# Performance work log

Hardware: AMD Instinct MI355X
Metric: run time of the kernel (lower is better)

Reference implementation:

```python
import jax, jax.numpy as jnp
import numpy as np

N = 100000   # occupied voxels
C = 128      # input_dim
G = 64       # voxel grid extent per axis


def _build_neighbor_map(rng):
    # random unique voxel coords in a G^3 grid + hash lookup for 3x3x3 offsets
    lin = rng.choice(G ** 3, size=N, replace=False)
    coords = np.stack(np.unravel_index(lin, (G, G, G)), axis=1).astype(np.int64)  # [N,3]
    lut = np.full(G ** 3, -1, np.int32)
    lut[lin] = np.arange(N, dtype=np.int32)
    o = np.arange(-1, 2)
    offs = np.stack(np.meshgrid(o, o, o, indexing='ij'), -1).reshape(27, 3)  # [27,3]
    nc = coords[None, :, :] + offs[:, None, :]                 # [27,N,3]
    valid = ((nc >= 0) & (nc < G)).all(-1)                     # [27,N]
    nlin = (nc[..., 0] * G + nc[..., 1]) * G + nc[..., 2]
    nbr = np.where(valid, lut[np.clip(nlin, 0, G ** 3 - 1)], -1).astype(np.int32)
    return nbr


def setup_inputs() -> dict:
    rng = np.random.default_rng(0)
    nbr = _build_neighbor_map(rng)
    key = jax.random.key(0)
    ks = jax.random.split(key, 5)
    h = C // 2
    x = jax.random.normal(ks[0], (N, C), jnp.float32)
    w1 = jax.random.normal(ks[1], (C, C), jnp.float32) * 0.05
    b1 = jnp.zeros((C,), jnp.float32)
    w2 = jax.random.normal(ks[2], (C, C), jnp.float32) * 0.05
    b2 = jnp.zeros((C,), jnp.float32)
    rw1 = jax.random.normal(ks[3], (27, h, h), jnp.float32) * 0.05
    rb1 = jnp.zeros((h,), jnp.float32)
    rw2 = jax.random.normal(ks[4], (27, h, h), jnp.float32) * 0.05
    rb2 = jnp.zeros((h,), jnp.float32)
    return dict(x=x, w1=w1, b1=b1, w2=w2, b2=b2,
                rw1=rw1, rb1=rb1, rw2=rw2, rb2=rb2,
                nbr=jnp.asarray(nbr))


def _sconv3(feat, nbr, W, b):
    # sparse 3x3x3 conv: gather neighbor features per kernel offset, GEMM, sum
    mask = (nbr >= 0).astype(feat.dtype)                  # [27,N]
    g = feat[jnp.maximum(nbr, 0)] * mask[:, :, None]      # [27,N,c]
    return jnp.einsum('knc,kcd->nd', g, W) + b            # [N,c]


def reference(x, w1, b1, w2, b2, rw1, rb1, rw2, rb2, nbr):
    h = x.shape[1] // 2
    y = x @ w1 + b1                                       # conv1 (1x1x1)
    conv_x, trans_x = y[:, :h], y[:, h:]                  # split
    # resblock (stride 1 -> no skip conv): relu(conv)->relu(conv) + identity
    r = jax.nn.relu(_sconv3(conv_x, nbr, rw1, rb1))
    r = jax.nn.relu(_sconv3(r, nbr, rw2, rb2))
    conv_x = (r + conv_x) + conv_x                        # resblock(x) + x
    # CodedVTRBlock source unavailable: modeled as identity on trans branch
    res = jnp.concatenate([conv_x, trans_x], axis=1) @ w2 + b2  # conv2 (1x1x1)
    return x + res
```

## Files before the change

### kernel.cpp

```cpp
#include <hip/hip_runtime.h>


#define N_PTS 100000
#define NBLK64 1563

typedef __attribute__((ext_vector_type(8))) short frag_ab;
typedef __attribute__((ext_vector_type(4))) float f32x4;
#define ZFRAG frag_ab{0, 0, 0, 0, 0, 0, 0, 0}

__device__ __forceinline__ unsigned short f2bf(float f) {
  union { float f; unsigned int i; } v; v.f = f;
  unsigned int r = v.i + 0x7fffu + ((v.i >> 16) & 1u);
  return (unsigned short)(r >> 16);
}
__device__ __forceinline__ float bf2f(unsigned short u) {
  union { unsigned int i; float f; } v; v.i = ((unsigned int)u) << 16; return v.f;
}

__device__ __forceinline__ void gload_lds16(const unsigned short* g, unsigned short* l) {
  __builtin_amdgcn_global_load_lds(
      (const __attribute__((address_space(1))) unsigned int*)g,
      (__attribute__((address_space(3))) unsigned int*)(unsigned int)(size_t)l,
      16, 0, 0);
}

__global__ __launch_bounds__(256) void k_prep(
    const float* __restrict__ w1, const float* __restrict__ w2,
    const float* __restrict__ rw1, const float* __restrict__ rw2,
    unsigned short* __restrict__ w1T, unsigned short* __restrict__ w2T,
    unsigned short* __restrict__ rw1T, unsigned short* __restrict__ rw2T) {
  int t = blockIdx.x * 256 + threadIdx.x;
  if (t < 128 * 128) {
    int c = t >> 7, d = t & 127;
    int pos = d * 128 + ((((c >> 3) ^ (d & 15)) << 3) | (c & 7));
    w1T[pos] = f2bf(w1[t]);
    w2T[pos] = f2bf(w2[t]);
  }
  if (t < 27 * 64 * 64) {
    int k = t >> 12, r = t & 4095, c = r >> 6, d = r & 63;
    int pos = (k << 12) + d * 64 + ((((c >> 3) ^ (d & 7)) << 3) | (c & 7));
    rw1T[pos] = f2bf(rw1[t]);
    rw2T[pos] = f2bf(rw2[t]);
  }
}

__global__ __launch_bounds__(256) void k_gemm_in(
    const float* __restrict__ x, const unsigned short* __restrict__ w1T,
    const float* __restrict__ b1, unsigned short* __restrict__ y) {
  __shared__ unsigned short sw[16384];
  const int tid = threadIdx.x, lane = tid & 63, w = tid >> 6;
  const int m16 = lane & 15, q = lane >> 4;
#pragma unroll
  for (int r = 0; r < 8; ++r) {
    const int off = (w * 8 + r) * 512 + lane * 8;
    gload_lds16(w1T + off, &sw[off]);
  }
  __syncthreads();
  const int rowbase = blockIdx.x * 64 + w * 16;
  const int r0 = rowbase + m16;
  const int rc = r0 < N_PTS ? r0 : N_PTS - 1;
  f32x4 acc[8] = {};
#pragma unroll
  for (int kk = 0; kk < 4; ++kk) {
    const float* xp = x + (size_t)rc * 128 + kk * 32 + q * 8;
    float4 f0 = *(const float4*)xp;
    float4 f1 = *(const float4*)(xp + 4);
    frag_ab a;
    a[0] = (short)f2bf(f0.x); a[1] = (short)f2bf(f0.y);
    a[2] = (short)f2bf(f0.z); a[3] = (short)f2bf(f0.w);
    a[4] = (short)f2bf(f1.x); a[5] = (short)f2bf(f1.y);
    a[6] = (short)f2bf(f1.z); a[7] = (short)f2bf(f1.w);
#pragma unroll
    for (int ct = 0; ct < 8; ++ct) {
      const int d = ct * 16 + m16;
      const int phys = ((kk << 2) | q) ^ m16;
      frag_ab bf = *(const frag_ab*)(&sw[d * 128 + phys * 8]);
      acc[ct] = __builtin_amdgcn_mfma_f32_16x16x32_bf16(a, bf, acc[ct], 0, 0, 0);
    }
  }
#pragma unroll
  for (int ct = 0; ct < 8; ++ct) {
    const int col = ct * 16 + m16;
    const float bias = b1[col];
#pragma unroll
    for (int j = 0; j < 4; ++j) {
      int r = rowbase + q * 4 + j;
      if (r < N_PTS) y[(size_t)r * 128 + col] = f2bf(acc[ct][j] + bias);
    }
  }
}

template <bool FUSE>
__global__ __launch_bounds__(256) void k_conv(
    const unsigned short* __restrict__ feat, const int fstride,
    const int* __restrict__ nbr,
    const unsigned short* __restrict__ rwT, const float* __restrict__ rb,
    const unsigned short* __restrict__ res, unsigned short* __restrict__ out) {
  __shared__ unsigned short sw[2][4096];
  const int tid = threadIdx.x, lane = tid & 63, w = tid >> 6;
  const int m16 = lane & 15, q = lane >> 4;
  const int rowbase = blockIdx.x * 64 + w * 16;
  const int p0 = rowbase + m16;
  const bool v0 = p0 < N_PTS;
  const int s0 = w * 1024 + lane * 8;
  const int s1 = s0 + 512;

  int i0r[2];
  i0r[0] = v0 ? nbr[p0] : -1;
  i0r[1] = v0 ? nbr[N_PTS + p0] : -1;

  frag_ab A[2][2];
#pragma unroll
  for (int a = 0; a < 2; ++a)
#pragma unroll
    for (int c = 0; c < 2; ++c) A[a][c] = ZFRAG;

  {
    gload_lds16(rwT + s0, &sw[0][s0]);
    gload_lds16(rwT + s1, &sw[0][s1]);
    if (i0r[0] >= 0) {
      const unsigned short* fp = feat + (size_t)i0r[0] * fstride + q * 8;
      A[0][0] = *(const frag_ab*)fp; A[0][1] = *(const frag_ab*)(fp + 32);
    }
  }
  __syncthreads();

  f32x4 acc[4] = {};
#pragma unroll
  for (int k = 0; k < 27; ++k) {
    const int b = k & 1;
    if (k + 1 < 27) {
      const unsigned short* src = rwT + ((k + 1) << 12);
      gload_lds16(src + s0, &sw[b ^ 1][s0]);
      gload_lds16(src + s1, &sw[b ^ 1][s1]);
      const int n = (k + 1) & 1;
      int j0 = i0r[n];
      A[n][0] = ZFRAG; A[n][1] = ZFRAG;
      if (j0 >= 0) {
        const unsigned short* fp = feat + (size_t)j0 * fstride + q * 8;
        A[n][0] = *(const frag_ab*)fp; A[n][1] = *(const frag_ab*)(fp + 32);
      }
    }
    if (k + 2 < 27) {
      i0r[k & 1] = v0 ? nbr[(k + 2) * N_PTS + p0] : -1;
    }
#pragma unroll
    for (int kk = 0; kk < 2; ++kk)
#pragma unroll
      for (int ct = 0; ct < 4; ++ct) {
        const int d = ct * 16 + m16;
        const int phys = ((kk << 2) | q) ^ (m16 & 7);
        frag_ab bf = *(const frag_ab*)(&sw[b][d * 64 + phys * 8]);
        acc[ct] = __builtin_amdgcn_mfma_f32_16x16x32_bf16(A[b][kk], bf, acc[ct], 0, 0, 0);
      }
    __syncthreads();
  }

#pragma unroll
  for (int ct = 0; ct < 4; ++ct) {
    const int col = ct * 16 + m16;
    const float bias = rb[col];
#pragma unroll
    for (int j = 0; j < 4; ++j) {
      const int r = rowbase + q * 4 + j;
      if (r < N_PTS) {
        float v = acc[ct][j] + bias;
        v = v > 0.f ? v : 0.f;
        if constexpr (FUSE) v += 2.f * bf2f(res[(size_t)r * 128 + col]);
        out[(size_t)r * 64 + col] = f2bf(v);
      }
    }
  }
}

__global__ __launch_bounds__(256) void k_gemm_out(
    const float* __restrict__ x, const unsigned short* __restrict__ z1,
    const unsigned short* __restrict__ y, const unsigned short* __restrict__ w2T,
    const float* __restrict__ b2, float* __restrict__ out) {
  __shared__ unsigned short sw[16384];
  const int tid = threadIdx.x, lane = tid & 63, w = tid >> 6;
  const int m16 = lane & 15, q = lane >> 4;
#pragma unroll
  for (int r = 0; r < 8; ++r) {
    const int off = (w * 8 + r) * 512 + lane * 8;
    gload_lds16(w2T + off, &sw[off]);
  }
  __syncthreads();
  const int rowbase = blockIdx.x * 64 + w * 16;
  const int r0 = rowbase + m16;
  const int rc = r0 < N_PTS ? r0 : N_PTS - 1;
  f32x4 acc[8] = {};
#pragma unroll
  for (int kk = 0; kk < 4; ++kk) {
    const unsigned short* ap = (kk < 2)
        ? (z1 + (size_t)rc * 64 + kk * 32 + q * 8)
        : (y + (size_t)rc * 128 + 64 + (kk - 2) * 32 + q * 8);
    frag_ab a = *(const frag_ab*)ap;
#pragma unroll
    for (int ct = 0; ct < 8; ++ct) {
      const int d = ct * 16 + m16;
      const int phys = ((kk << 2) | q) ^ m16;
      frag_ab bf = *(const frag_ab*)(&sw[d * 128 + phys * 8]);
      acc[ct] = __builtin_amdgcn_mfma_f32_16x16x32_bf16(a, bf, acc[ct], 0, 0, 0);
    }
  }
#pragma unroll
  for (int ct = 0; ct < 8; ++ct) {
    const int col = ct * 16 + m16;
    const float bias = b2[col];
#pragma unroll
    for (int j = 0; j < 4; ++j) {
      int r = rowbase + q * 4 + j;
      if (r < N_PTS) {
        size_t o = (size_t)r * 128 + col;
        out[o] = acc[ct][j] + bias + x[o];
      }
    }
  }
}

extern "C" void kernel_launch(void* const* d_in, const int* in_sizes, int n_in,
                              void* d_out, int out_size, void* d_ws, size_t ws_size,
                              hipStream_t stream) {
  const float* x   = (const float*)d_in[0];
  const float* w1  = (const float*)d_in[1];
  const float* b1  = (const float*)d_in[2];
  const float* w2  = (const float*)d_in[3];
  const float* b2  = (const float*)d_in[4];
  const float* rw1 = (const float*)d_in[5];
  const float* rb1 = (const float*)d_in[6];
  const float* rw2 = (const float*)d_in[7];
  const float* rb2 = (const float*)d_in[8];
  const int* nbr = (const int*)d_in[9];
  float* out = (float*)d_out;

  char* ws = (char*)d_ws;
  unsigned short* w1T  = (unsigned short*)(ws);
  unsigned short* w2T  = (unsigned short*)(ws + 32768);
  unsigned short* rw1T = (unsigned short*)(ws + 65536);
  unsigned short* rw2T = (unsigned short*)(ws + 286720);
  unsigned short* y    = (unsigned short*)(ws + 507904);
  unsigned short* r1   = (unsigned short*)(ws + 507904 + 25600000);
  unsigned short* z1   = (unsigned short*)(ws + 507904 + 38400000);

  k_prep<<<432, 256, 0, stream>>>(w1, w2, rw1, rw2, w1T, w2T, rw1T, rw2T);
  k_gemm_in<<<NBLK64, 256, 0, stream>>>(x, w1T, b1, y);
  k_conv<false><<<NBLK64, 256, 0, stream>>>(y, 128, nbr, rw1T, rb1, nullptr, r1);
  k_conv<true><<<NBLK64, 256, 0, stream>>>(r1, 64, nbr, rw2T, rb2, y, z1);
  k_gemm_out<<<NBLK64, 256, 0, stream>>>(x, z1, y, w2T, b2, out);
}
```

Baseline: 254.5 us.

## Restructure sparse conv as single-wave 64x64 register tiles with deep prefetch

The sparse conv kernels drop LDS staging and block-wide barriers. Each 64-thread wave now computes a 64-row by 64-column tile, loading the per-offset weight fragments straight from global memory into registers and reusing each one across 4 row tiles. Neighbor indices are prefetched 5 offsets ahead and feature gathers and weights are double-buffered one offset ahead. The weight prep no longer swizzles. The aim is to remove the per-offset __syncthreads and raise MFMA work per weight load, at the cost of higher register pressure, lower occupancy (64 threads per block, 1563 blocks) and uncoalesced weight reads from L2.

```diff
diff --git a/kernel.cpp b/kernel.cpp
--- a/kernel.cpp
+++ b/kernel.cpp
@@ -38,7 +38,7 @@
   }
   if (t < 27 * 64 * 64) {
     int k = t >> 12, r = t & 4095, c = r >> 6, d = r & 63;
-    int pos = (k << 12) + d * 64 + ((((c >> 3) ^ (d & 7)) << 3) | (c & 7));
+    int pos = (k << 12) + d * 64 + c;
     rw1T[pos] = f2bf(rw1[t]);
     rw2T[pos] = f2bf(rw2[t]);
   }
@@ -90,86 +90,114 @@
   }
 }
 
+__device__ __forceinline__ void conv_loadI(int I[4], const int* nbr, int kc,
+                                           const int p[4], const bool v[4]) {
+#pragma unroll
+  for (int rt = 0; rt < 4; ++rt)
+    I[rt] = v[rt] ? nbr[(size_t)kc * N_PTS + p[rt]] : -1;
+}
+
+__device__ __forceinline__ void conv_loadB(frag_ab B[4][2],
+                                           const unsigned short* wk,
+                                           int m16, int q) {
+#pragma unroll
+  for (int ct = 0; ct < 4; ++ct)
+#pragma unroll
+    for (int kk = 0; kk < 2; ++kk)
+      B[ct][kk] = *(const frag_ab*)(wk + (ct * 16 + m16) * 64 + kk * 32 + q * 8);
+}
+
+__device__ __forceinline__ void conv_gatherA(frag_ab A[4][2], const int I[4],
+                                             const unsigned short* feat,
+                                             int fstride, int q) {
+#pragma unroll
+  for (int rt = 0; rt < 4; ++rt) {
+    A[rt][0] = ZFRAG; A[rt][1] = ZFRAG;
+    if (I[rt] >= 0) {
+      const unsigned short* fp = feat + (size_t)I[rt] * fstride + q * 8;
+      A[rt][0] = *(const frag_ab*)fp;
+      A[rt][1] = *(const frag_ab*)(fp + 32);
+    }
+  }
+}
+
+__device__ __forceinline__ void conv_mfma(f32x4 acc[4][4], const frag_ab A[4][2],
+                                          const frag_ab B[4][2]) {
+#pragma unroll
+  for (int kk = 0; kk < 2; ++kk)
+#pragma unroll
+    for (int rt = 0; rt < 4; ++rt)
+#pragma unroll
+      for (int ct = 0; ct < 4; ++ct)
+        acc[rt][ct] =
+            __builtin_amdgcn_mfma_f32_16x16x32_bf16(A[rt][kk], B[ct][kk], acc[rt][ct], 0, 0, 0);
+}
+
 template <bool FUSE>
-__global__ __launch_bounds__(256) void k_conv(
+__global__ __launch_bounds__(64, 2) void k_conv(
     const unsigned short* __restrict__ feat, const int fstride,
     const int* __restrict__ nbr,
     const unsigned short* __restrict__ rwT, const float* __restrict__ rb,
     const unsigned short* __restrict__ res, unsigned short* __restrict__ out) {
-  __shared__ unsigned short sw[2][4096];
-  const int tid = threadIdx.x, lane = tid & 63, w = tid >> 6;
+  const int lane = threadIdx.x & 63;
   const int m16 = lane & 15, q = lane >> 4;
-  const int rowbase = blockIdx.x * 64 + w * 16;
-  const int p0 = rowbase + m16;
-  const bool v0 = p0 < N_PTS;
-  const int s0 = w * 1024 + lane * 8;
-  const int s1 = s0 + 512;
-
-  int i0r[2];
-  i0r[0] = v0 ? nbr[p0] : -1;
-  i0r[1] = v0 ? nbr[N_PTS + p0] : -1;
-
-  frag_ab A[2][2];
-#pragma unroll
-  for (int a = 0; a < 2; ++a)
-#pragma unroll
-    for (int c = 0; c < 2; ++c) A[a][c] = ZFRAG;
-
-  {
-    gload_lds16(rwT + s0, &sw[0][s0]);
-    gload_lds16(rwT + s1, &sw[0][s1]);
-    if (i0r[0] >= 0) {
-      const unsigned short* fp = feat + (size_t)i0r[0] * fstride + q * 8;
-      A[0][0] = *(const frag_ab*)fp; A[0][1] = *(const frag_ab*)(fp + 32);
-    }
-  }
-  __syncthreads();
-
-  f32x4 acc[4] = {};
-#pragma unroll
-  for (int k = 0; k < 27; ++k) {
-    const int b = k & 1;
-    if (k + 1 < 27) {
-      const unsigned short* src = rwT + ((k + 1) << 12);
-      gload_lds16(src + s0, &sw[b ^ 1][s0]);
-      gload_lds16(src + s1, &sw[b ^ 1][s1]);
-      const int n = (k + 1) & 1;
-      int j0 = i0r[n];
-      A[n][0] = ZFRAG; A[n][1] = ZFRAG;
-      if (j0 >= 0) {
-        const unsigned short* fp = feat + (size_t)j0 * fstride + q * 8;
-        A[n][0] = *(const frag_ab*)fp; A[n][1] = *(const frag_ab*)(fp + 32);
-      }
-    }
-    if (k + 2 < 27) {
-      i0r[k & 1] = v0 ? nbr[(k + 2) * N_PTS + p0] : -1;
-    }
-#pragma unroll
-    for (int kk = 0; kk < 2; ++kk)
-#pragma unroll
-      for (int ct = 0; ct < 4; ++ct) {
-        const int d = ct * 16 + m16;
-        const int phys = ((kk << 2) | q) ^ (m16 & 7);
-        frag_ab bf = *(const frag_ab*)(&sw[b][d * 64 + phys * 8]);
-        acc[ct] = __builtin_amdgcn_mfma_f32_16x16x32_bf16(A[b][kk], bf, acc[ct], 0, 0, 0);
-      }
-    __syncthreads();
-  }
+  const int rowbase = blockIdx.x * 64;
+
+  int p[4]; bool v[4];
+#pragma unroll
+  for (int rt = 0; rt < 4; ++rt) {
+    p[rt] = rowbase + rt * 16 + m16;
+    v[rt] = p[rt] < N_PTS;
+  }
+
+  int I[6][4];
+  frag_ab A[2][4][2];
+  frag_ab B[2][4][2];
+  f32x4 acc[4][4] = {};
+
+  conv_loadI(I[0], nbr, 0, p, v);
+  conv_loadI(I[1], nbr, 1, p, v);
+  conv_loadI(I[2], nbr, 2, p, v);
+  conv_loadI(I[3], nbr, 3, p, v);
+  conv_loadI(I[4], nbr, 4, p, v);
+  conv_loadB(B[0], rwT, m16, q);
+  conv_gatherA(A[0], I[0], feat, fstride, q);
+
+  for (int k0 = 0; k0 < 24; k0 += 6) {
+#pragma unroll
+    for (int u = 0; u < 6; ++u) {
+      const int k = k0 + u;
+      const int kc = (k + 5 < 27) ? k + 5 : 26;
+      conv_loadI(I[(u + 5) % 6], nbr, kc, p, v);
+      conv_loadB(B[(u + 1) & 1], rwT + ((size_t)(k + 1) << 12), m16, q);
+      conv_gatherA(A[(u + 1) & 1], I[(u + 1) % 6], feat, fstride, q);
+      conv_mfma(acc, A[u & 1], B[u & 1]);
+    }
+  }
+  conv_loadB(B[1], rwT + ((size_t)25 << 12), m16, q);
+  conv_gatherA(A[1], I[25 % 6], feat, fstride, q);
+  conv_mfma(acc, A[0], B[0]);
+  conv_loadB(B[0], rwT + ((size_t)26 << 12), m16, q);
+  conv_gatherA(A[0], I[26 % 6], feat, fstride, q);
+  conv_mfma(acc, A[1], B[1]);
+  conv_mfma(acc, A[0], B[0]);
 
 #pragma unroll
   for (int ct = 0; ct < 4; ++ct) {
     const int col = ct * 16 + m16;
     const float bias = rb[col];
 #pragma unroll
-    for (int j = 0; j < 4; ++j) {
-      const int r = rowbase + q * 4 + j;
-      if (r < N_PTS) {
-        float v = acc[ct][j] + bias;
-        v = v > 0.f ? v : 0.f;
-        if constexpr (FUSE) v += 2.f * bf2f(res[(size_t)r * 128 + col]);
-        out[(size_t)r * 64 + col] = f2bf(v);
+    for (int rt = 0; rt < 4; ++rt)
+#pragma unroll
+      for (int j = 0; j < 4; ++j) {
+        const int r = rowbase + rt * 16 + q * 4 + j;
+        if (r < N_PTS) {
+          float vv = acc[rt][ct][j] + bias;
+          vv = vv > 0.f ? vv : 0.f;
+          if constexpr (FUSE) vv += 2.f * bf2f(res[(size_t)r * 128 + col]);
+          out[(size_t)r * 64 + col] = f2bf(vv);
+        }
       }
-    }
   }
 }
 
@@ -245,7 +273,7 @@
 
   k_prep<<<432, 256, 0, stream>>>(w1, w2, rw1, rw2, w1T, w2T, rw1T, rw2T);
   k_gemm_in<<<NBLK64, 256, 0, stream>>>(x, w1T, b1, y);
-  k_conv<false><<<NBLK64, 256, 0, stream>>>(y, 128, nbr, rw1T, rb1, nullptr, r1);
-  k_conv<true><<<NBLK64, 256, 0, stream>>>(r1, 64, nbr, rw2T, rb2, y, z1);
+  k_conv<false><<<NBLK64, 64, 0, stream>>>(y, 128, nbr, rw1T, rb1, nullptr, r1);
+  k_conv<true><<<NBLK64, 64, 0, stream>>>(r1, 64, nbr, rw2T, rb2, y, z1);
   k_gemm_out<<<NBLK64, 256, 0, stream>>>(x, z1, y, w2T, b2, out);
 }
```

New measurement: 308.0 us. +21.0%, slower.

## Deepen sparse-conv pipeline and process 128 rows per block

Applied to the files above, without the earlier changes.

The sparse conv kernel now handles two 16-row tiles per wave (128 rows per block), so each LDS weight tile is reused twice as often. Weight staging uses a 4-deep LDS ring with prefetch two offsets ahead. Neighbor indices are loaded three offsets ahead, and feature gathers are issued unconditionally with masking applied at compute time. Explicit vmcnt waits and raw s_barrier replace __syncthreads to overlap gathers with MFMA work. In exchange it uses more registers and LDS and launches half as many blocks, which may reduce occupancy.

```diff
diff --git a/kernel.cpp b/kernel.cpp
--- a/kernel.cpp
+++ b/kernel.cpp
@@ -3,6 +3,7 @@
 
 #define N_PTS 100000
 #define NBLK64 1563
+#define NBLK128 782
 
 typedef __attribute__((ext_vector_type(8))) short frag_ab;
 typedef __attribute__((ext_vector_type(4))) float f32x4;
@@ -96,80 +97,127 @@
     const int* __restrict__ nbr,
     const unsigned short* __restrict__ rwT, const float* __restrict__ rb,
     const unsigned short* __restrict__ res, unsigned short* __restrict__ out) {
-  __shared__ unsigned short sw[2][4096];
+  __shared__ unsigned short sw[4][4096];
   const int tid = threadIdx.x, lane = tid & 63, w = tid >> 6;
   const int m16 = lane & 15, q = lane >> 4;
-  const int rowbase = blockIdx.x * 64 + w * 16;
-  const int p0 = rowbase + m16;
-  const bool v0 = p0 < N_PTS;
+  const int rowbase = blockIdx.x * 128 + w * 32;
+  const int p0 = rowbase + m16, p1 = p0 + 16;
+  const bool v0 = p0 < N_PTS, v1 = p1 < N_PTS;
+  const int pc0 = v0 ? p0 : N_PTS - 1, pc1 = v1 ? p1 : N_PTS - 1;
   const int s0 = w * 1024 + lane * 8;
   const int s1 = s0 + 512;
 
-  int i0r[2];
-  i0r[0] = v0 ? nbr[p0] : -1;
-  i0r[1] = v0 ? nbr[N_PTS + p0] : -1;
-
-  frag_ab A[2][2];
-#pragma unroll
-  for (int a = 0; a < 2; ++a)
-#pragma unroll
-    for (int c = 0; c < 2; ++c) A[a][c] = ZFRAG;
+  int I[4][2];
+  int im[2][2];
+  frag_ab A[2][2][2];
+  f32x4 acc[2][4] = {};
+
+#define CONV_GATHER(slot, isrc)                                                 \
+  {                                                                             \
+    const int i0 = v0 ? (isrc)[0] : -1;                                         \
+    const int i1 = v1 ? (isrc)[1] : -1;                                         \
+    im[slot][0] = i0; im[slot][1] = i1;                                         \
+    const size_t j0 = (size_t)(i0 < 0 ? 0 : i0);                                \
+    const size_t j1 = (size_t)(i1 < 0 ? 0 : i1);                                \
+    const unsigned short* f0 = feat + j0 * fstride + q * 8;                     \
+    const unsigned short* f1 = feat + j1 * fstride + q * 8;                     \
+    A[slot][0][0] = *(const frag_ab*)f0; A[slot][0][1] = *(const frag_ab*)(f0 + 32); \
+    A[slot][1][0] = *(const frag_ab*)f1; A[slot][1][1] = *(const frag_ab*)(f1 + 32); \
+  }
+
+#define CONV_COMPUTE(buf, slot)                                                 \
+  {                                                                             \
+    frag_ab Ac[2][2];                                                           \
+    _Pragma("unroll") for (int rt = 0; rt < 2; ++rt)                            \
+      _Pragma("unroll") for (int kk = 0; kk < 2; ++kk) {                        \
+        frag_ab a = A[slot][rt][kk];                                            \
+        if (im[slot][rt] < 0) a = ZFRAG;                                        \
+        Ac[rt][kk] = a;                                                         \
+      }                                                                         \
+    _Pragma("unroll") for (int kk = 0; kk < 2; ++kk)                            \
+      _Pragma("unroll") for (int ct = 0; ct < 4; ++ct) {                        \
+        const int d = ct * 16 + m16;                                            \
+        const int phys = ((kk << 2) | q) ^ (m16 & 7);                           \
+        frag_ab bf = *(const frag_ab*)(&sw[buf][d * 64 + phys * 8]);            \
+        acc[0][ct] = __builtin_amdgcn_mfma_f32_16x16x32_bf16(Ac[0][kk], bf, acc[0][ct], 0, 0, 0); \
+        acc[1][ct] = __builtin_amdgcn_mfma_f32_16x16x32_bf16(Ac[1][kk], bf, acc[1][ct], 0, 0, 0); \
+      }                                                                         \
+  }
+
+  gload_lds16(rwT + s0, &sw[0][s0]);
+  gload_lds16(rwT + s1, &sw[0][s1]);
+  gload_lds16(rwT + 4096 + s0, &sw[1][s0]);
+  gload_lds16(rwT + 4096 + s1, &sw[1][s1]);
+#pragma unroll
+  for (int s = 0; s < 3; ++s) {
+    I[s][0] = nbr[(size_t)s * N_PTS + pc0];
+    I[s][1] = nbr[(size_t)s * N_PTS + pc1];
+  }
+  CONV_GATHER(0, I[0]);
+  __builtin_amdgcn_s_barrier();
+
+  for (int k0 = 0; k0 < 24; k0 += 4) {
+#pragma unroll
+    for (int u = 0; u < 4; ++u) {
+      const int k = k0 + u;
+      const int cur = u & 1, nxt = cur ^ 1;
+      {
+        const unsigned short* src = rwT + ((size_t)(k + 2) << 12);
+        unsigned short* dst = sw[(u + 2) & 3];
+        gload_lds16(src + s0, dst + s0);
+        gload_lds16(src + s1, dst + s1);
+      }
+      I[(u + 3) & 3][0] = nbr[(size_t)(k + 3) * N_PTS + pc0];
+      I[(u + 3) & 3][1] = nbr[(size_t)(k + 3) * N_PTS + pc1];
+      CONV_GATHER(nxt, I[(u + 1) & 3]);
+      asm volatile("s_waitcnt vmcnt(8)" ::: "memory");
+      __builtin_amdgcn_sched_barrier(0);
+      CONV_COMPUTE(u & 3, cur);
+      __builtin_amdgcn_s_barrier();
+    }
+  }
 
   {
-    gload_lds16(rwT + s0, &sw[0][s0]);
-    gload_lds16(rwT + s1, &sw[0][s1]);
-    if (i0r[0] >= 0) {
-      const unsigned short* fp = feat + (size_t)i0r[0] * fstride + q * 8;
-      A[0][0] = *(const frag_ab*)fp; A[0][1] = *(const frag_ab*)(fp + 32);
-    }
-  }
-  __syncthreads();
-
-  f32x4 acc[4] = {};
-#pragma unroll
-  for (int k = 0; k < 27; ++k) {
-    const int b = k & 1;
-    if (k + 1 < 27) {
-      const unsigned short* src = rwT + ((k + 1) << 12);
-      gload_lds16(src + s0, &sw[b ^ 1][s0]);
-      gload_lds16(src + s1, &sw[b ^ 1][s1]);
-      const int n = (k + 1) & 1;
-      int j0 = i0r[n];
-      A[n][0] = ZFRAG; A[n][1] = ZFRAG;
-      if (j0 >= 0) {
-        const unsigned short* fp = feat + (size_t)j0 * fstride + q * 8;
-        A[n][0] = *(const frag_ab*)fp; A[n][1] = *(const frag_ab*)(fp + 32);
-      }
-    }
-    if (k + 2 < 27) {
-      i0r[k & 1] = v0 ? nbr[(k + 2) * N_PTS + p0] : -1;
-    }
-#pragma unroll
-    for (int kk = 0; kk < 2; ++kk)
-#pragma unroll
-      for (int ct = 0; ct < 4; ++ct) {
-        const int d = ct * 16 + m16;
-        const int phys = ((kk << 2) | q) ^ (m16 & 7);
-        frag_ab bf = *(const frag_ab*)(&sw[b][d * 64 + phys * 8]);
-        acc[ct] = __builtin_amdgcn_mfma_f32_16x16x32_bf16(A[b][kk], bf, acc[ct], 0, 0, 0);
-      }
-    __syncthreads();
-  }
+    const unsigned short* src = rwT + ((size_t)26 << 12);
+    gload_lds16(src + s0, &sw[2][s0]);
+    gload_lds16(src + s1, &sw[2][s1]);
+    CONV_GATHER(1, I[1]);
+    asm volatile("s_waitcnt vmcnt(6)" ::: "memory");
+    __builtin_amdgcn_sched_barrier(0);
+    CONV_COMPUTE(0, 0);
+    __builtin_amdgcn_s_barrier();
+  }
+  {
+    CONV_GATHER(0, I[2]);
+    asm volatile("s_waitcnt vmcnt(4)" ::: "memory");
+    __builtin_amdgcn_sched_barrier(0);
+    CONV_COMPUTE(1, 1);
+    __builtin_amdgcn_s_barrier();
+  }
+  {
+    asm volatile("s_waitcnt vmcnt(0)" ::: "memory");
+    __builtin_amdgcn_sched_barrier(0);
+    CONV_COMPUTE(2, 0);
+  }
+#undef CONV_GATHER
+#undef CONV_COMPUTE
 
 #pragma unroll
   for (int ct = 0; ct < 4; ++ct) {
     const int col = ct * 16 + m16;
     const float bias = rb[col];
 #pragma unroll
-    for (int j = 0; j < 4; ++j) {
-      const int r = rowbase + q * 4 + j;
-      if (r < N_PTS) {
-        float v = acc[ct][j] + bias;
-        v = v > 0.f ? v : 0.f;
-        if constexpr (FUSE) v += 2.f * bf2f(res[(size_t)r * 128 + col]);
-        out[(size_t)r * 64 + col] = f2bf(v);
+    for (int rt = 0; rt < 2; ++rt)
+#pragma unroll
+      for (int j = 0; j < 4; ++j) {
+        const int r = rowbase + rt * 16 + q * 4 + j;
+        if (r < N_PTS) {
+          float v = acc[rt][ct][j] + bias;
+          v = v > 0.f ? v : 0.f;
+          if constexpr (FUSE) v += 2.f * bf2f(res[(size_t)r * 128 + col]);
+          out[(size_t)r * 64 + col] = f2bf(v);
+        }
       }
-    }
   }
 }
 
@@ -245,7 +293,7 @@
 
   k_prep<<<432, 256, 0, stream>>>(w1, w2, rw1, rw2, w1T, w2T, rw1T, rw2T);
   k_gemm_in<<<NBLK64, 256, 0, stream>>>(x, w1T, b1, y);
-  k_conv<false><<<NBLK64, 256, 0, stream>>>(y, 128, nbr, rw1T, rb1, nullptr, r1);
-  k_conv<true><<<NBLK64, 256, 0, stream>>>(r1, 64, nbr, rw2T, rb2, y, z1);
+  k_conv<false><<<NBLK128, 256, 0, stream>>>(y, 128, nbr, rw1T, rb1, nullptr, r1);
+  k_conv<true><<<NBLK128, 256, 0, stream>>>(r1, 64, nbr, rw2T, rb2, y, z1);
   k_gemm_out<<<NBLK64, 256, 0, stream>>>(x, z1, y, w2T, b2, out);
 }
```

Result: slower. 275.3 us (+8.2%).
